# Kernel optimization log

Hardware: AMD Instinct MI355X
Metric: run time of the kernel (lower is better)

## Reference

```python
import jax, jax.numpy as jnp
import numpy as np

P = 200000   # num_paths
C = 50000    # num_channels
K = 8        # channels per path (fixed-width neighbor list)
F = 32       # feat_dim
ITERS = 5    # num_iterations


def setup_inputs() -> dict:
    key = jax.random.key(0)
    ks = jax.random.split(key, 12)
    s = 1.0 / np.sqrt(F)

    def u(k, shape):
        return jax.random.uniform(k, shape, jnp.float32, -s, s)

    return {
        "paths": jax.random.normal(ks[0], (P, F), jnp.float32),
        "channels": jax.random.normal(ks[1], (C, F), jnp.float32),
        "path_to_channel": jax.random.randint(ks[2], (P, K), 0, C),
        "W_ih1": u(ks[3], (3 * F, F)),
        "W_hh1": u(ks[4], (3 * F, F)),
        "b_ih1": u(ks[5], (3 * F,)),
        "b_hh1": u(ks[6], (3 * F,)),
        "W_ih2": u(ks[7], (3 * F, F)),
        "W_hh2": u(ks[8], (3 * F, F)),
        "b_ih2": u(ks[9], (3 * F,)),
        "b_hh2": u(ks[10], (3 * F,)),
    }


def gru_cell(x, h, W_ih, W_hh, b_ih, b_hh):
    # torch.nn.GRUCell math
    gi = x @ W_ih.T + b_ih          # [N, 3F]
    gh = h @ W_hh.T + b_hh          # [N, 3F]
    i_r, i_z, i_n = jnp.split(gi, 3, axis=-1)
    h_r, h_z, h_n = jnp.split(gh, 3, axis=-1)
    r = jax.nn.sigmoid(i_r + h_r)
    z = jax.nn.sigmoid(i_z + h_z)
    n = jnp.tanh(i_n + r * h_n)
    return (1.0 - z) * n + z * h


def reference(paths, channels, path_to_channel,
              W_ih1, W_hh1, b_ih1, b_hh1,
              W_ih2, W_hh2, b_ih2, b_hh2):
    num_channels = channels.shape[0]
    h_p, h_c = paths, channels
    idx_flat = path_to_channel.reshape(-1)      # [P*K], row-major (p0k0, p0k1, ...)
    steps = path_to_channel.T                   # [K, P]
    k_per_path = path_to_channel.shape[1]

    for _ in range(ITERS):
        # path update: sequentially fold each path's channel list through GRU1
        h_c_cur = h_c

        def step(hp, idx):
            return gru_cell(h_c_cur[idx], hp, W_ih1, W_hh1, b_ih1, b_hh1), None

        h_p, _ = jax.lax.scan(step, h_p, steps)
        # channel update: sum of incident path states, one GRU2 step
        edge_feats = jnp.repeat(h_p, k_per_path, axis=0)  # [P*K, F]
        agg = jax.ops.segment_sum(edge_feats, idx_flat, num_segments=num_channels)
        h_c = gru_cell(agg, h_c, W_ih2, W_hh2, b_ih2, b_hh2)

    return h_p, h_c
```

## Files before the change

kernel.cpp:

```cpp
#include <hip/hip_runtime.h>

#define FD 32
#define KNB 8
#define NITER 5
#define NCH 256

typedef __bf16 bf16x8 __attribute__((ext_vector_type(8)));
typedef float  f32x4  __attribute__((ext_vector_type(4)));

__device__ __forceinline__ float frcp_(float a) { return __builtin_amdgcn_rcpf(a); }
__device__ __forceinline__ float fexp2_(float a) { return __builtin_amdgcn_exp2f(a); }
__device__ __forceinline__ float sigmoidf_(float a) {
    return frcp_(1.0f + fexp2_(a * -1.44269504f));
}
__device__ __forceinline__ float tanhf_(float a) {
    return 1.0f - 2.0f * frcp_(fexp2_(a * 2.88539009f) + 1.0f);
}


__global__ __launch_bounds__(256) void bincount_kernel(
    const int* __restrict__ p2c, int* __restrict__ cnt1, int E, int NR)
{
    __shared__ int lds[256];
    int b = blockIdx.x;
    int per = (E + NCH - 1) / NCH;
    int s0 = b * per, s1 = s0 + per; if (s1 > E) s1 = E;
    int t = threadIdx.x;
    if (t < NR) lds[t] = 0;
    __syncthreads();
    for (int e = s0 + t; e < s1; e += 256)
        atomicAdd(&lds[p2c[e] >> 8], 1);
    __syncthreads();
    if (t < NR) cnt1[(size_t)b * NR + t] = lds[t];
}

__global__ __launch_bounds__(256) void scan_chunks_kernel(
    int* __restrict__ cnt1, int* __restrict__ bstart, int NR, int E)
{
    __shared__ int tt[256];
    int t = threadIdx.x;
    int tot = 0;
    if (t < NR)
        for (int b = 0; b < NCH; b++) tot += cnt1[(size_t)b * NR + t];
    tt[t] = (t < NR) ? tot : 0;
    __syncthreads();
    for (int d = 1; d < 256; d <<= 1) {
        int v = (t >= d) ? tt[t - d] : 0;
        __syncthreads();
        tt[t] += v;
        __syncthreads();
    }
    if (t < NR) {
        int run = (t == 0) ? 0 : tt[t - 1];
        bstart[t] = run;
        for (int b = 0; b < NCH; b++) {
            int v = cnt1[(size_t)b * NR + t];
            cnt1[(size_t)b * NR + t] = run;
            run += v;
        }
        if (t == NR - 1) bstart[NR] = E;
    }
}

__global__ __launch_bounds__(256) void binfill_kernel(
    const int* __restrict__ p2c, const int* __restrict__ cnt1,
    int2* __restrict__ ebuf, int E, int NR)
{
    __shared__ int cur[256];
    int b = blockIdx.x;
    int per = (E + NCH - 1) / NCH;
    int s0 = b * per, s1 = s0 + per; if (s1 > E) s1 = E;
    int t = threadIdx.x;
    if (t < NR) cur[t] = cnt1[(size_t)b * NR + t];
    __syncthreads();
    for (int e = s0 + t; e < s1; e += 256) {
        int ch = p2c[e];
        int slot = atomicAdd(&cur[ch >> 8], 1);
        ebuf[slot] = make_int2(e >> 3, ch);
    }
}

__global__ __launch_bounds__(256) void buckscan_kernel(
    const int2* __restrict__ ebuf, const int* __restrict__ bstart,
    int* __restrict__ offsets, int* __restrict__ bsum, int C)
{
    __shared__ int h[256];
    __shared__ int sc[256];
    int r = blockIdx.x;
    int t = threadIdx.x;
    h[t] = 0;
    __syncthreads();
    int s0 = bstart[r], s1 = bstart[r + 1];
    for (int i = s0 + t; i < s1; i += 256)
        atomicAdd(&h[ebuf[i].y & 255], 1);
    __syncthreads();
    int mine = h[t];
    sc[t] = mine;
    __syncthreads();
    #pragma unroll
    for (int d = 1; d < 256; d <<= 1) {
        int v = (t >= d) ? sc[t - d] : 0;
        __syncthreads();
        sc[t] += v;
        __syncthreads();
    }
    int c = (r << 8) + t;
    if (c < C) offsets[c] = sc[t] - mine;
    if (t == 255) bsum[r] = sc[255];
}

__global__ __launch_bounds__(256) void scan_bsums_kernel(
    const int* __restrict__ bsum, int* __restrict__ bbase,
    int* __restrict__ offsets, int NR, int C, int E)
{
    __shared__ int sc[256];
    int t = threadIdx.x;
    int mine = (t < NR) ? bsum[t] : 0;
    sc[t] = mine;
    __syncthreads();
    #pragma unroll
    for (int d = 1; d < 256; d <<= 1) {
        int v = (t >= d) ? sc[t - d] : 0;
        __syncthreads();
        sc[t] += v;
        __syncthreads();
    }
    if (t < NR) bbase[t] = sc[t] - mine;
    if (t == 0) offsets[C] = E;
}

__global__ __launch_bounds__(256) void addback_kernel(
    int* __restrict__ offsets, const int* __restrict__ bbase, int C)
{
    int c = blockIdx.x * blockDim.x + threadIdx.x;
    if (c < C) offsets[c] += bbase[c >> 8];
}

__global__ __launch_bounds__(256) void buckfill_kernel(
    const int2* __restrict__ ebuf, const int* __restrict__ bstart,
    const int* __restrict__ offsets, int* __restrict__ elist, int C)
{
    __shared__ int cur[256];
    int r = blockIdx.x;
    int t = threadIdx.x;
    int c = (r << 8) + t;
    cur[t] = (c < C) ? offsets[c] : 0;
    __syncthreads();
    int s0 = bstart[r], s1 = bstart[r + 1];
    for (int i = s0 + t; i < s1; i += 256) {
        int2 v = ebuf[i];
        int slot = atomicAdd(&cur[v.y & 255], 1);
        elist[slot] = v.x;
    }
}


__global__ __launch_bounds__(256) void hc_init_kernel(
    const float* __restrict__ src, float* __restrict__ h_c,
    __bf16* __restrict__ dst, int n8)
{
    int i = blockIdx.x * blockDim.x + threadIdx.x;
    if (i >= n8) return;
    const float4* s = (const float4*)(src + (size_t)i * 8);
    float4 u = s[0], v = s[1];
    float4* d = (float4*)(h_c + (size_t)i * 8);
    d[0] = u; d[1] = v;
    bf16x8 o;
    o[0]=(__bf16)u.x; o[1]=(__bf16)u.y; o[2]=(__bf16)u.z; o[3]=(__bf16)u.w;
    o[4]=(__bf16)v.x; o[5]=(__bf16)v.y; o[6]=(__bf16)v.z; o[7]=(__bf16)v.w;
    ((bf16x8*)dst)[i] = o;
}

__global__ __launch_bounds__(256) void wconv_kernel(
    const float* __restrict__ W1i, const float* __restrict__ W1h,
    const float* __restrict__ W2i, const float* __restrict__ W2h,
    __bf16* __restrict__ w1x, __bf16* __restrict__ w1h,
    __bf16* __restrict__ w2xH, __bf16* __restrict__ w2xL,
    __bf16* __restrict__ w2hH, __bf16* __restrict__ w2hL)
{
    int i = blockIdx.x * blockDim.x + threadIdx.x;
    if (i >= 96 * FD) return;
    w1x[i] = (__bf16)W1i[i];
    w1h[i] = (__bf16)W1h[i];
    float c = W2i[i]; __bf16 ch = (__bf16)c;
    w2xH[i] = ch; w2xL[i] = (__bf16)(c - (float)ch);
    float d = W2h[i]; __bf16 dh = (__bf16)d;
    w2hH[i] = dh; w2hL[i] = (__bf16)(d - (float)dh);
}

#define HLP 40
__global__ __launch_bounds__(256) void path_fused_kernel(
    float* __restrict__ h_p, const int* __restrict__ p2c,
    const __bf16* __restrict__ hcb,
    const __bf16* __restrict__ w1x, const __bf16* __restrict__ w1h,
    const float* __restrict__ bih, const float* __restrict__ bhh,
    __bf16* __restrict__ hpb, int ntiles)
{
    __shared__ __bf16 hl[64][HLP];
    const int tid  = threadIdx.x;
    const int wid  = tid >> 6;
    const int lane = tid & 63;
    const int c    = lane & 15;
    const int kg   = lane >> 4;

    bf16x8 Bx[6], Bh[6];
    #pragma unroll
    for (int t = 0; t < 6; t++) {
        Bx[t] = *(const bf16x8*)(w1x + (size_t)(16*t + c) * FD + 8*kg);
        Bh[t] = *(const bf16x8*)(w1h + (size_t)(16*t + c) * FD + 8*kg);
    }
    f32x4 cin_rz[4], cin_xn[2], cin_hn[2];
    #pragma unroll
    for (int t = 0; t < 4; t++) {
        float b = bih[16*t + c] + bhh[16*t + c];
        cin_rz[t] = (f32x4){b, b, b, b};
    }
    #pragma unroll
    for (int fi = 0; fi < 2; fi++) {
        float bi = bih[64 + 16*fi + c];
        float bh = bhh[64 + 16*fi + c];
        cin_xn[fi] = (f32x4){bi, bi, bi, bi};
        cin_hn[fi] = (f32x4){bh, bh, bh, bh};
    }

    for (int tile = blockIdx.x; tile < ntiles; tile += gridDim.x) {
        const int blk0 = tile * 64;
        const int rbase = blk0 + wid*16 + 4*kg;

        float hD[8];
        #pragma unroll
        for (int q = 0; q < 4; q++)
            #pragma unroll
            for (int fi = 0; fi < 2; fi++) {
                float v = h_p[(size_t)(rbase + q) * FD + c + 16*fi];
                hD[2*q + fi] = v;
                hl[wid*16 + 4*kg + q][c + 16*fi] = (__bf16)v;
            }

        const int pA = blk0 + wid*16 + c;
        const int4* pp = (const int4*)(p2c + (size_t)pA * KNB);
        int4 ia = pp[0], ib = pp[1];
        int idxA[KNB] = {ia.x, ia.y, ia.z, ia.w, ib.x, ib.y, ib.z, ib.w};
        bf16x8 Ax[KNB];
        #pragma unroll
        for (int k = 0; k < KNB; k++)
            Ax[k] = *(const bf16x8*)(hcb + (size_t)idxA[k] * FD + 8*kg);

        const int rowA = wid*16 + c;
        #pragma unroll
        for (int k = 0; k < KNB; k++) {
            bf16x8 Ah = *(const bf16x8*)&hl[rowA][8*kg];

            f32x4 arz[4], xn[2], hn[2];
            #pragma unroll
            for (int t = 0; t < 4; t++) {
                arz[t] = __builtin_amdgcn_mfma_f32_16x16x32_bf16(Ax[k], Bx[t], cin_rz[t], 0, 0, 0);
                arz[t] = __builtin_amdgcn_mfma_f32_16x16x32_bf16(Ah,    Bh[t], arz[t],   0, 0, 0);
            }
            #pragma unroll
            for (int fi = 0; fi < 2; fi++) {
                xn[fi] = __builtin_amdgcn_mfma_f32_16x16x32_bf16(Ax[k], Bx[4+fi], cin_xn[fi], 0, 0, 0);
                hn[fi] = __builtin_amdgcn_mfma_f32_16x16x32_bf16(Ah,    Bh[4+fi], cin_hn[fi], 0, 0, 0);
            }

            #pragma unroll
            for (int q = 0; q < 4; q++)
                #pragma unroll
                for (int fi = 0; fi < 2; fi++) {
                    float r = sigmoidf_(arz[fi][q]);
                    float z = sigmoidf_(arz[2+fi][q]);
                    float n = tanhf_(fmaf(r, hn[fi][q], xn[fi][q]));
                    float ho = hD[2*q + fi];
                    float hv = fmaf(z, ho - n, n);
                    hD[2*q + fi] = hv;
                    hl[wid*16 + 4*kg + q][c + 16*fi] = (__bf16)hv;
                }
        }

        #pragma unroll
        for (int q = 0; q < 4; q++)
            #pragma unroll
            for (int fi = 0; fi < 2; fi++)
                h_p[(size_t)(rbase + q) * FD + c + 16*fi] = hD[2*q + fi];

        __syncthreads();
        {
            int r  = tid >> 2;
            int c0 = (tid & 3) * 8;
            bf16x8 o = *(const bf16x8*)&hl[r][c0];
            *(bf16x8*)(hpb + ((size_t)(blk0 + r)) * FD + c0) = o;
        }
        __syncthreads();
    }
}

__global__ __launch_bounds__(256) void gchannel_kernel(
    const __bf16* __restrict__ hpb, const int* __restrict__ offsets,
    const int* __restrict__ elist, float* __restrict__ h_c,
    const __bf16* __restrict__ w2xH, const __bf16* __restrict__ w2xL,
    const __bf16* __restrict__ w2hH, const __bf16* __restrict__ w2hL,
    const float* __restrict__ bih, const float* __restrict__ bhh,
    __bf16* __restrict__ hcb, int C)
{
    const int tid  = threadIdx.x;
    const int wid  = tid >> 6;
    const int lane = tid & 63;
    const int c    = lane & 15;
    const int kg   = lane >> 4;
    const int blk0 = blockIdx.x * 64;
    const int chA  = blk0 + wid*16 + c;

    float xr[8];
    #pragma unroll
    for (int j = 0; j < 8; j++) xr[j] = 0.f;
    int s = 0, e = 0;
    if (chA < C) { s = offsets[chA]; e = offsets[chA + 1]; }
    int i = s;
    for (; i + 2 <= e; i += 2) {
        int e0 = elist[i], e1 = elist[i + 1];
        bf16x8 v0 = *(const bf16x8*)(hpb + (size_t)e0 * FD + 8*kg);
        bf16x8 v1 = *(const bf16x8*)(hpb + (size_t)e1 * FD + 8*kg);
        #pragma unroll
        for (int j = 0; j < 8; j++) xr[j] += (float)v0[j] + (float)v1[j];
    }
    if (i < e) {
        bf16x8 v0 = *(const bf16x8*)(hpb + (size_t)elist[i] * FD + 8*kg);
        #pragma unroll
        for (int j = 0; j < 8; j++) xr[j] += (float)v0[j];
    }

    float hr[8];
    if (chA < C) {
        const float4* ha = (const float4*)(h_c + (size_t)chA * FD + 8*kg);
        float4 h0 = ha[0], h1 = ha[1];
        hr[0]=h0.x; hr[1]=h0.y; hr[2]=h0.z; hr[3]=h0.w;
        hr[4]=h1.x; hr[5]=h1.y; hr[6]=h1.z; hr[7]=h1.w;
    } else {
        #pragma unroll
        for (int j = 0; j < 8; j++) hr[j] = 0.f;
    }
    bf16x8 AxH, AxL, AhH, AhL;
    #pragma unroll
    for (int j = 0; j < 8; j++) {
        __bf16 xh = (__bf16)xr[j]; AxH[j] = xh; AxL[j] = (__bf16)(xr[j] - (float)xh);
        __bf16 hh = (__bf16)hr[j]; AhH[j] = hh; AhL[j] = (__bf16)(hr[j] - (float)hh);
    }

    f32x4 cin_rz[4], cin_xn[2], cin_hn[2];
    #pragma unroll
    for (int t = 0; t < 4; t++) {
        float b = bih[16*t + c] + bhh[16*t + c];
        cin_rz[t] = (f32x4){b, b, b, b};
    }
    #pragma unroll
    for (int fi = 0; fi < 2; fi++) {
        float bi = bih[64 + 16*fi + c];
        float bh = bhh[64 + 16*fi + c];
        cin_xn[fi] = (f32x4){bi, bi, bi, bi};
        cin_hn[fi] = (f32x4){bh, bh, bh, bh};
    }

    f32x4 arz[4], xn[2], hn[2];
    #pragma unroll
    for (int t = 0; t < 4; t++) {
        size_t wo = (size_t)(16*t + c) * FD + 8*kg;
        bf16x8 BxH_ = *(const bf16x8*)(w2xH + wo);
        bf16x8 BxL_ = *(const bf16x8*)(w2xL + wo);
        bf16x8 BhH_ = *(const bf16x8*)(w2hH + wo);
        bf16x8 BhL_ = *(const bf16x8*)(w2hL + wo);
        f32x4 a = cin_rz[t];
        a = __builtin_amdgcn_mfma_f32_16x16x32_bf16(AxH, BxH_, a, 0, 0, 0);
        a = __builtin_amdgcn_mfma_f32_16x16x32_bf16(AxH, BxL_, a, 0, 0, 0);
        a = __builtin_amdgcn_mfma_f32_16x16x32_bf16(AxL, BxH_, a, 0, 0, 0);
        a = __builtin_amdgcn_mfma_f32_16x16x32_bf16(AhH, BhH_, a, 0, 0, 0);
        a = __builtin_amdgcn_mfma_f32_16x16x32_bf16(AhH, BhL_, a, 0, 0, 0);
        a = __builtin_amdgcn_mfma_f32_16x16x32_bf16(AhL, BhH_, a, 0, 0, 0);
        arz[t] = a;
    }
    #pragma unroll
    for (int fi = 0; fi < 2; fi++) {
        size_t wo = (size_t)(16*(4+fi) + c) * FD + 8*kg;
        bf16x8 BxH_ = *(const bf16x8*)(w2xH + wo);
        bf16x8 BxL_ = *(const bf16x8*)(w2xL + wo);
        bf16x8 BhH_ = *(const bf16x8*)(w2hH + wo);
        bf16x8 BhL_ = *(const bf16x8*)(w2hL + wo);
        f32x4 a = cin_xn[fi];
        a = __builtin_amdgcn_mfma_f32_16x16x32_bf16(AxH, BxH_, a, 0, 0, 0);
        a = __builtin_amdgcn_mfma_f32_16x16x32_bf16(AxH, BxL_, a, 0, 0, 0);
        a = __builtin_amdgcn_mfma_f32_16x16x32_bf16(AxL, BxH_, a, 0, 0, 0);
        xn[fi] = a;
        f32x4 b = cin_hn[fi];
        b = __builtin_amdgcn_mfma_f32_16x16x32_bf16(AhH, BhH_, b, 0, 0, 0);
        b = __builtin_amdgcn_mfma_f32_16x16x32_bf16(AhH, BhL_, b, 0, 0, 0);
        b = __builtin_amdgcn_mfma_f32_16x16x32_bf16(AhL, BhH_, b, 0, 0, 0);
        hn[fi] = b;
    }

    #pragma unroll
    for (int q = 0; q < 4; q++) {
        int row = blk0 + wid*16 + 4*kg + q;
        if (row < C) {
            #pragma unroll
            for (int fi = 0; fi < 2; fi++) {
                float r = sigmoidf_(arz[fi][q]);
                float z = sigmoidf_(arz[2+fi][q]);
                float n = tanhf_(fmaf(r, hn[fi][q], xn[fi][q]));
                float ho = h_c[(size_t)row * FD + c + 16*fi];
                float hv = fmaf(z, ho - n, n);
                h_c[(size_t)row * FD + c + 16*fi] = hv;
                hcb[(size_t)row * FD + c + 16*fi] = (__bf16)hv;
            }
        }
    }
}


__global__ __launch_bounds__(256) void path_update_kernel(
    const float* __restrict__ h_c, float* __restrict__ h_p,
    const int* __restrict__ p2c,
    const float* __restrict__ Wih, const float* __restrict__ Whh,
    const float* __restrict__ bih, const float* __restrict__ bhh, int P)
{
    int p = blockIdx.x * blockDim.x + threadIdx.x;
    if (p >= P) return;

    float h[FD];
    const float4* hp4 = (const float4*)(h_p + (size_t)p * FD);
    #pragma unroll
    for (int i = 0; i < FD / 4; i++) {
        float4 v = hp4[i];
        h[4*i] = v.x; h[4*i+1] = v.y; h[4*i+2] = v.z; h[4*i+3] = v.w;
    }

    int idx[KNB];
    const int4* pi = (const int4*)(p2c + (size_t)p * KNB);
    int4 i0 = pi[0], i1 = pi[1];
    idx[0]=i0.x; idx[1]=i0.y; idx[2]=i0.z; idx[3]=i0.w;
    idx[4]=i1.x; idx[5]=i1.y; idx[6]=i1.z; idx[7]=i1.w;

    for (int k = 0; k < KNB; k++) {
        float x[FD];
        const float4* xr = (const float4*)(h_c + (size_t)idx[k] * FD);
        #pragma unroll
        for (int i = 0; i < FD / 4; i++) {
            float4 v = xr[i];
            x[4*i] = v.x; x[4*i+1] = v.y; x[4*i+2] = v.z; x[4*i+3] = v.w;
        }

        float hn[FD];
        #pragma unroll 4
        for (int j = 0; j < FD; j++) {
            float air = bih[j],        ahr = bhh[j];
            float aiz = bih[FD + j],   ahz = bhh[FD + j];
            float ain = bih[2*FD + j], ahn = bhh[2*FD + j];
            #pragma unroll
            for (int i = 0; i < FD; i++) {
                air = fmaf(Wih[j*FD + i],          x[i], air);
                ahr = fmaf(Whh[j*FD + i],          h[i], ahr);
                aiz = fmaf(Wih[(FD + j)*FD + i],   x[i], aiz);
                ahz = fmaf(Whh[(FD + j)*FD + i],   h[i], ahz);
                ain = fmaf(Wih[(2*FD + j)*FD + i], x[i], ain);
                ahn = fmaf(Whh[(2*FD + j)*FD + i], h[i], ahn);
            }
            float r = sigmoidf_(air + ahr);
            float z = sigmoidf_(aiz + ahz);
            float n = tanhf_(ain + r * ahn);
            hn[j] = (1.0f - z) * n + z * h[j];
        }
        #pragma unroll
        for (int j = 0; j < FD; j++) h[j] = hn[j];
    }

    float4* hpw = (float4*)(h_p + (size_t)p * FD);
    #pragma unroll
    for (int i = 0; i < FD / 4; i++) {
        float4 v;
        v.x = h[4*i]; v.y = h[4*i+1]; v.z = h[4*i+2]; v.w = h[4*i+3];
        hpw[i] = v;
    }
}

__global__ __launch_bounds__(256) void scatter_agg_atomic_kernel(
    const float* __restrict__ h_p, const int* __restrict__ p2c,
    float* __restrict__ agg, int P)
{
    int p = blockIdx.x * blockDim.x + threadIdx.x;
    if (p >= P) return;
    const float* hr = h_p + (size_t)p * FD;
    #pragma unroll
    for (int k = 0; k < KNB; k++) {
        int c = p2c[(size_t)p * KNB + k];
        float* ar = agg + (size_t)c * FD;
        #pragma unroll
        for (int i = 0; i < FD; i++) atomicAdd(ar + i, hr[i]);
    }
}

__global__ __launch_bounds__(256) void channel_update_kernel(
    const float* __restrict__ agg, float* __restrict__ h_c,
    const float* __restrict__ Wih, const float* __restrict__ Whh,
    const float* __restrict__ bih, const float* __restrict__ bhh, int C)
{
    int c = blockIdx.x * blockDim.x + threadIdx.x;
    if (c >= C) return;

    float h[FD], x[FD];
    const float4* hr = (const float4*)(h_c + (size_t)c * FD);
    const float4* xr = (const float4*)(agg + (size_t)c * FD);
    #pragma unroll
    for (int i = 0; i < FD / 4; i++) {
        float4 v = hr[i];
        h[4*i] = v.x; h[4*i+1] = v.y; h[4*i+2] = v.z; h[4*i+3] = v.w;
        float4 w = xr[i];
        x[4*i] = w.x; x[4*i+1] = w.y; x[4*i+2] = w.z; x[4*i+3] = w.w;
    }

    float hn[FD];
    #pragma unroll 4
    for (int j = 0; j < FD; j++) {
        float air = bih[j],        ahr = bhh[j];
        float aiz = bih[FD + j],   ahz = bhh[FD + j];
        float ain = bih[2*FD + j], ahn = bhh[2*FD + j];
        #pragma unroll
        for (int i = 0; i < FD; i++) {
            air = fmaf(Wih[j*FD + i],          x[i], air);
            ahr = fmaf(Whh[j*FD + i],          h[i], ahr);
            aiz = fmaf(Wih[(FD + j)*FD + i],   x[i], aiz);
            ahz = fmaf(Whh[(FD + j)*FD + i],   h[i], ahz);
            ain = fmaf(Wih[(2*FD + j)*FD + i], x[i], ain);
            ahn = fmaf(Whh[(2*FD + j)*FD + i], h[i], ahn);
        }
        float r = sigmoidf_(air + ahr);
        float z = sigmoidf_(aiz + ahz);
        float n = tanhf_(ain + r * ahn);
        hn[j] = (1.0f - z) * n + z * h[j];
    }

    float4* hw = (float4*)(h_c + (size_t)c * FD);
    #pragma unroll
    for (int i = 0; i < FD / 4; i++) {
        float4 v;
        v.x = hn[4*i]; v.y = hn[4*i+1]; v.z = hn[4*i+2]; v.w = hn[4*i+3];
        hw[i] = v;
    }
}

extern "C" void kernel_launch(void* const* d_in, const int* in_sizes, int n_in,
                              void* d_out, int out_size, void* d_ws, size_t ws_size,
                              hipStream_t stream) {
    const float* paths    = (const float*)d_in[0];
    const float* channels = (const float*)d_in[1];
    const int*   p2c      = (const int*)d_in[2];
    const float* Wih1 = (const float*)d_in[3];
    const float* Whh1 = (const float*)d_in[4];
    const float* bih1 = (const float*)d_in[5];
    const float* bhh1 = (const float*)d_in[6];
    const float* Wih2 = (const float*)d_in[7];
    const float* Whh2 = (const float*)d_in[8];
    const float* bih2 = (const float*)d_in[9];
    const float* bhh2 = (const float*)d_in[10];

    const int P = in_sizes[0] / FD;
    const int C = in_sizes[1] / FD;
    const int E = P * KNB;
    const int NR = (C + 255) >> 8;

    float* h_p = (float*)d_out;
    float* h_c = h_p + (size_t)P * FD;

    char* ws = (char*)d_ws;
    size_t bs_off  = 0;
    size_t ofs_off = (bs_off + (size_t)(2 * NR) * 4 + 255) & ~(size_t)255;
    size_t bst_off = (ofs_off + (size_t)(C + 1) * 4 + 255) & ~(size_t)255;
    size_t el_off  = (bst_off + (size_t)(NR + 1) * 4 + 255) & ~(size_t)255;
    size_t hcb_off = (el_off + (size_t)E * 4 + 255) & ~(size_t)255;
    size_t wb_off  = (hcb_off + (size_t)C * FD * 2 + 255) & ~(size_t)255;
    size_t wmat_b  = (size_t)96 * FD * 2;
    size_t uni_off = (wb_off + 6 * wmat_b + 255) & ~(size_t)255;
    size_t ebuf_b  = (size_t)E * 8;
    size_t cnt1_b  = (size_t)NCH * NR * 4;
    size_t hpb_b   = (size_t)P * FD * 2;
    size_t bld_b   = ebuf_b + cnt1_b;
    size_t uni_b   = (hpb_b > bld_b) ? hpb_b : bld_b;

    int*    bsum    = (int*)(ws + bs_off);
    int*    bbase   = bsum + NR;
    int*    offsets = (int*)(ws + ofs_off);
    int*    bstart  = (int*)(ws + bst_off);
    int*    elist   = (int*)(ws + el_off);
    __bf16* hcb     = (__bf16*)(ws + hcb_off);
    __bf16* w1x     = (__bf16*)(ws + wb_off);
    __bf16* w1h     = (__bf16*)(ws + wb_off + 1 * wmat_b);
    __bf16* w2xH    = (__bf16*)(ws + wb_off + 2 * wmat_b);
    __bf16* w2xL    = (__bf16*)(ws + wb_off + 3 * wmat_b);
    __bf16* w2hH    = (__bf16*)(ws + wb_off + 4 * wmat_b);
    __bf16* w2hL    = (__bf16*)(ws + wb_off + 5 * wmat_b);
    int2*   ebuf    = (int2*)(ws + uni_off);
    int*    cnt1    = (int*)(ws + uni_off + ebuf_b);
    __bf16* hpb     = (__bf16*)(ws + uni_off);

    const bool mfma_ok = (P % 64 == 0) && (C <= 65536);
    const bool tier1 = mfma_ok && (ws_size >= uni_off + uni_b);

    dim3 pb(256), pg((P + 255) / 256);
    dim3 cb(256), cg((C + 255) / 256);

    if (tier1) {
        hipMemcpyAsync(h_p, paths, (size_t)P * FD * sizeof(float),
                       hipMemcpyDeviceToDevice, stream);
        int n8 = C * FD / 8;
        hc_init_kernel<<<(n8 + 255) / 256, 256, 0, stream>>>(channels, h_c, hcb, n8);
        wconv_kernel<<<(96 * FD + 255) / 256, 256, 0, stream>>>(
            Wih1, Whh1, Wih2, Whh2, w1x, w1h, w2xH, w2xL, w2hH, w2hL);

        bincount_kernel<<<NCH, 256, 0, stream>>>(p2c, cnt1, E, NR);
        scan_chunks_kernel<<<1, 256, 0, stream>>>(cnt1, bstart, NR, E);
        binfill_kernel<<<NCH, 256, 0, stream>>>(p2c, cnt1, ebuf, E, NR);
        buckscan_kernel<<<NR, 256, 0, stream>>>(ebuf, bstart, offsets, bsum, C);
        scan_bsums_kernel<<<1, 256, 0, stream>>>(bsum, bbase, offsets, NR, C, E);
        addback_kernel<<<cg, cb, 0, stream>>>(offsets, bbase, C);
        buckfill_kernel<<<NR, 256, 0, stream>>>(ebuf, bstart, offsets, elist, C);

        const int ntiles = P / 64;
        int pgrid = ntiles < 1024 ? ntiles : 1024;
        dim3 xg((C + 63) / 64), xb(256);
        for (int it = 0; it < NITER; it++) {
            path_fused_kernel<<<pgrid, 256, 0, stream>>>(h_p, p2c, hcb,
                                                         w1x, w1h, bih1, bhh1,
                                                         hpb, ntiles);
            gchannel_kernel<<<xg, xb, 0, stream>>>(hpb, offsets, elist, h_c,
                                                   w2xH, w2xL, w2hH, w2hL,
                                                   bih2, bhh2, hcb, C);
        }
    } else {
        float* agg0 = (float*)d_ws;
        size_t aggf_b = (size_t)C * FD * sizeof(float);
        hipMemcpyAsync(h_p, paths, (size_t)P * FD * sizeof(float),
                       hipMemcpyDeviceToDevice, stream);
        hipMemcpyAsync(h_c, channels, (size_t)C * FD * sizeof(float),
                       hipMemcpyDeviceToDevice, stream);
        for (int it = 0; it < NITER; it++) {
            path_update_kernel<<<pg, pb, 0, stream>>>(h_c, h_p, p2c,
                                                      Wih1, Whh1, bih1, bhh1, P);
            hipMemsetAsync(agg0, 0, aggf_b, stream);
            scatter_agg_atomic_kernel<<<pg, pb, 0, stream>>>(h_p, p2c, agg0, P);
            channel_update_kernel<<<cg, cb, 0, stream>>>(agg0, h_c,
                                                         Wih2, Whh2, bih2, bhh2, C);
        }
    }
}
```

Baseline: 558.0 us.

## Interleave two path tiles per block and unroll channel gather by four

The path kernel drops its grid-stride loop and has each block handle two 64-path tiles. The GRU steps of the two tiles are interleaved, so the MFMA and transcendental work of one tile can hide the latency of the other's serial dependency chain. The channel gather loop is unrolled to four edges with two accumulators to put more loads in flight. The cost is higher register pressure and a larger grid, which may lower occupancy.

```diff
diff --git a/kernel.cpp b/kernel.cpp
--- a/kernel.cpp
+++ b/kernel.cpp
@@ -189,6 +189,35 @@
 }
 
 #define HLP 40
+
+#define GRU_STEP(hl_, hD_, Axk_)                                               \
+    {                                                                          \
+        bf16x8 Ah = *(const bf16x8*)&hl_[rowA][8*kg];                          \
+        f32x4 arz[4], xn[2], hn[2];                                            \
+        _Pragma("unroll")                                                      \
+        for (int t = 0; t < 4; t++) {                                          \
+            arz[t] = __builtin_amdgcn_mfma_f32_16x16x32_bf16(Axk_, Bx[t], cin_rz[t], 0, 0, 0); \
+            arz[t] = __builtin_amdgcn_mfma_f32_16x16x32_bf16(Ah,   Bh[t], arz[t],    0, 0, 0); \
+        }                                                                      \
+        _Pragma("unroll")                                                      \
+        for (int fi = 0; fi < 2; fi++) {                                       \
+            xn[fi] = __builtin_amdgcn_mfma_f32_16x16x32_bf16(Axk_, Bx[4+fi], cin_xn[fi], 0, 0, 0); \
+            hn[fi] = __builtin_amdgcn_mfma_f32_16x16x32_bf16(Ah,   Bh[4+fi], cin_hn[fi], 0, 0, 0); \
+        }                                                                      \
+        _Pragma("unroll")                                                      \
+        for (int q = 0; q < 4; q++)                                            \
+            _Pragma("unroll")                                                  \
+            for (int fi = 0; fi < 2; fi++) {                                   \
+                float r = sigmoidf_(arz[fi][q]);                               \
+                float z = sigmoidf_(arz[2+fi][q]);                             \
+                float n = tanhf_(fmaf(r, hn[fi][q], xn[fi][q]));               \
+                float ho = hD_[2*q + fi];                                      \
+                float hv = fmaf(z, ho - n, n);                                 \
+                hD_[2*q + fi] = hv;                                            \
+                hl_[wid*16 + 4*kg + q][c + 16*fi] = (__bf16)hv;                \
+            }                                                                  \
+    }
+
 __global__ __launch_bounds__(256) void path_fused_kernel(
     float* __restrict__ h_p, const int* __restrict__ p2c,
     const __bf16* __restrict__ hcb,
@@ -196,7 +225,8 @@
     const float* __restrict__ bih, const float* __restrict__ bhh,
     __bf16* __restrict__ hpb, int ntiles)
 {
-    __shared__ __bf16 hl[64][HLP];
+    __shared__ __bf16 hlA[64][HLP];
+    __shared__ __bf16 hlB[64][HLP];
     const int tid  = threadIdx.x;
     const int wid  = tid >> 6;
     const int lane = tid & 63;
@@ -223,74 +253,82 @@
         cin_hn[fi] = (f32x4){bh, bh, bh, bh};
     }
 
-    for (int tile = blockIdx.x; tile < ntiles; tile += gridDim.x) {
-        const int blk0 = tile * 64;
-        const int rbase = blk0 + wid*16 + 4*kg;
-
-        float hD[8];
+    const int tileA = blockIdx.x * 2;
+    const int tileB = tileA + 1;
+    const bool hasB = (tileB < ntiles);
+    const int blk0A = tileA * 64;
+    const int blk0B = tileB * 64;
+    const int rbaseA = blk0A + wid*16 + 4*kg;
+    const int rbaseB = blk0B + wid*16 + 4*kg;
+    const int rowA = wid*16 + c;
+
+    float hDA[8];
+    #pragma unroll
+    for (int q = 0; q < 4; q++)
+        #pragma unroll
+        for (int fi = 0; fi < 2; fi++) {
+            float v = h_p[(size_t)(rbaseA + q) * FD + c + 16*fi];
+            hDA[2*q + fi] = v;
+            hlA[wid*16 + 4*kg + q][c + 16*fi] = (__bf16)v;
+        }
+    const int pA = blk0A + wid*16 + c;
+    const int4* ppA = (const int4*)(p2c + (size_t)pA * KNB);
+    int4 iaA = ppA[0], ibA = ppA[1];
+    int idxA[KNB] = {iaA.x, iaA.y, iaA.z, iaA.w, ibA.x, ibA.y, ibA.z, ibA.w};
+    bf16x8 AxA[KNB];
+    #pragma unroll
+    for (int k = 0; k < KNB; k++)
+        AxA[k] = *(const bf16x8*)(hcb + (size_t)idxA[k] * FD + 8*kg);
+
+    float hDB[8];
+    bf16x8 AxB[KNB];
+    if (hasB) {
         #pragma unroll
         for (int q = 0; q < 4; q++)
             #pragma unroll
             for (int fi = 0; fi < 2; fi++) {
-                float v = h_p[(size_t)(rbase + q) * FD + c + 16*fi];
-                hD[2*q + fi] = v;
-                hl[wid*16 + 4*kg + q][c + 16*fi] = (__bf16)v;
+                float v = h_p[(size_t)(rbaseB + q) * FD + c + 16*fi];
+                hDB[2*q + fi] = v;
+                hlB[wid*16 + 4*kg + q][c + 16*fi] = (__bf16)v;
             }
-
-        const int pA = blk0 + wid*16 + c;
-        const int4* pp = (const int4*)(p2c + (size_t)pA * KNB);
-        int4 ia = pp[0], ib = pp[1];
-        int idxA[KNB] = {ia.x, ia.y, ia.z, ia.w, ib.x, ib.y, ib.z, ib.w};
-        bf16x8 Ax[KNB];
+        const int pB = blk0B + wid*16 + c;
+        const int4* ppB = (const int4*)(p2c + (size_t)pB * KNB);
+        int4 iaB = ppB[0], ibB = ppB[1];
+        int idxB[KNB] = {iaB.x, iaB.y, iaB.z, iaB.w, ibB.x, ibB.y, ibB.z, ibB.w};
         #pragma unroll
         for (int k = 0; k < KNB; k++)
-            Ax[k] = *(const bf16x8*)(hcb + (size_t)idxA[k] * FD + 8*kg);
-
-        const int rowA = wid*16 + c;
-        #pragma unroll
-        for (int k = 0; k < KNB; k++) {
-            bf16x8 Ah = *(const bf16x8*)&hl[rowA][8*kg];
-
-            f32x4 arz[4], xn[2], hn[2];
-            #pragma unroll
-            for (int t = 0; t < 4; t++) {
-                arz[t] = __builtin_amdgcn_mfma_f32_16x16x32_bf16(Ax[k], Bx[t], cin_rz[t], 0, 0, 0);
-                arz[t] = __builtin_amdgcn_mfma_f32_16x16x32_bf16(Ah,    Bh[t], arz[t],   0, 0, 0);
-            }
-            #pragma unroll
-            for (int fi = 0; fi < 2; fi++) {
-                xn[fi] = __builtin_amdgcn_mfma_f32_16x16x32_bf16(Ax[k], Bx[4+fi], cin_xn[fi], 0, 0, 0);
-                hn[fi] = __builtin_amdgcn_mfma_f32_16x16x32_bf16(Ah,    Bh[4+fi], cin_hn[fi], 0, 0, 0);
-            }
-
-            #pragma unroll
-            for (int q = 0; q < 4; q++)
-                #pragma unroll
-                for (int fi = 0; fi < 2; fi++) {
-                    float r = sigmoidf_(arz[fi][q]);
-                    float z = sigmoidf_(arz[2+fi][q]);
-                    float n = tanhf_(fmaf(r, hn[fi][q], xn[fi][q]));
-                    float ho = hD[2*q + fi];
-                    float hv = fmaf(z, ho - n, n);
-                    hD[2*q + fi] = hv;
-                    hl[wid*16 + 4*kg + q][c + 16*fi] = (__bf16)hv;
-                }
-        }
-
+            AxB[k] = *(const bf16x8*)(hcb + (size_t)idxB[k] * FD + 8*kg);
+    }
+
+    #pragma unroll
+    for (int k = 0; k < KNB; k++) {
+        GRU_STEP(hlA, hDA, AxA[k]);
+        if (hasB) GRU_STEP(hlB, hDB, AxB[k]);
+    }
+
+    #pragma unroll
+    for (int q = 0; q < 4; q++)
+        #pragma unroll
+        for (int fi = 0; fi < 2; fi++)
+            h_p[(size_t)(rbaseA + q) * FD + c + 16*fi] = hDA[2*q + fi];
+    if (hasB) {
         #pragma unroll
         for (int q = 0; q < 4; q++)
             #pragma unroll
             for (int fi = 0; fi < 2; fi++)
-                h_p[(size_t)(rbase + q) * FD + c + 16*fi] = hD[2*q + fi];
-
-        __syncthreads();
-        {
-            int r  = tid >> 2;
-            int c0 = (tid & 3) * 8;
-            bf16x8 o = *(const bf16x8*)&hl[r][c0];
-            *(bf16x8*)(hpb + ((size_t)(blk0 + r)) * FD + c0) = o;
-        }
-        __syncthreads();
+                h_p[(size_t)(rbaseB + q) * FD + c + 16*fi] = hDB[2*q + fi];
+    }
+
+    __syncthreads();
+    {
+        int r  = tid >> 2;
+        int c0 = (tid & 3) * 8;
+        bf16x8 oA = *(const bf16x8*)&hlA[r][c0];
+        *(bf16x8*)(hpb + ((size_t)(blk0A + r)) * FD + c0) = oA;
+        if (hasB) {
+            bf16x8 oB = *(const bf16x8*)&hlB[r][c0];
+            *(bf16x8*)(hpb + ((size_t)(blk0B + r)) * FD + c0) = oB;
+        }
     }
 }
 
@@ -310,24 +348,31 @@
     const int blk0 = blockIdx.x * 64;
     const int chA  = blk0 + wid*16 + c;
 
-    float xr[8];
-    #pragma unroll
-    for (int j = 0; j < 8; j++) xr[j] = 0.f;
+    float xr[8], xs[8];
+    #pragma unroll
+    for (int j = 0; j < 8; j++) { xr[j] = 0.f; xs[j] = 0.f; }
     int s = 0, e = 0;
     if (chA < C) { s = offsets[chA]; e = offsets[chA + 1]; }
     int i = s;
-    for (; i + 2 <= e; i += 2) {
-        int e0 = elist[i], e1 = elist[i + 1];
+    for (; i + 4 <= e; i += 4) {
+        int e0 = elist[i], e1 = elist[i + 1], e2 = elist[i + 2], e3 = elist[i + 3];
         bf16x8 v0 = *(const bf16x8*)(hpb + (size_t)e0 * FD + 8*kg);
         bf16x8 v1 = *(const bf16x8*)(hpb + (size_t)e1 * FD + 8*kg);
-        #pragma unroll
-        for (int j = 0; j < 8; j++) xr[j] += (float)v0[j] + (float)v1[j];
-    }
-    if (i < e) {
+        bf16x8 v2 = *(const bf16x8*)(hpb + (size_t)e2 * FD + 8*kg);
+        bf16x8 v3 = *(const bf16x8*)(hpb + (size_t)e3 * FD + 8*kg);
+        #pragma unroll
+        for (int j = 0; j < 8; j++) {
+            xr[j] += (float)v0[j] + (float)v2[j];
+            xs[j] += (float)v1[j] + (float)v3[j];
+        }
+    }
+    for (; i < e; i++) {
         bf16x8 v0 = *(const bf16x8*)(hpb + (size_t)elist[i] * FD + 8*kg);
         #pragma unroll
         for (int j = 0; j < 8; j++) xr[j] += (float)v0[j];
     }
+    #pragma unroll
+    for (int j = 0; j < 8; j++) xr[j] += xs[j];
 
     float hr[8];
     if (chA < C) {
@@ -622,7 +667,7 @@
         buckfill_kernel<<<NR, 256, 0, stream>>>(ebuf, bstart, offsets, elist, C);
 
         const int ntiles = P / 64;
-        int pgrid = ntiles < 1024 ? ntiles : 1024;
+        const int pgrid  = (ntiles + 1) / 2;
         dim3 xg((C + 63) / 64), xb(256);
         for (int it = 0; it < NITER; it++) {
             path_fused_kernel<<<pgrid, 256, 0, stream>>>(h_p, p2c, hcb,
```

Result: no change. 557.7 us (-0.0%).
